# Kernel optimization log

Measured on AMD Instinct MI355X. Metric: run time of the kernel, lower is better.

Reference implementation:

```python
import jax, jax.numpy as jnp
import numpy as np

B, S, D, H = 2, 2048, 1024, 16
DK = D // H
SOFTCAP = 30.0


def setup_inputs() -> dict:
    key = jax.random.key(0)
    ks = jax.random.split(key, 6)
    inp = jax.random.normal(ks[0], (B, S, D), dtype=jnp.float32)
    count_bias = jax.random.normal(ks[1], (B, 1, S, S), dtype=jnp.float32) * 0.1
    # causal boolean mask: True = allowed
    causal = jnp.tril(jnp.ones((S, S), dtype=bool))
    attn_mask = jnp.broadcast_to(causal[None, None, :, :], (B, 1, S, S))
    scale = 0.02
    Wq = jax.random.normal(ks[2], (D, D), dtype=jnp.float32) * scale
    Wk = jax.random.normal(ks[3], (D, D), dtype=jnp.float32) * scale
    Wv = jax.random.normal(ks[4], (D, D), dtype=jnp.float32) * scale
    Wo = jax.random.normal(ks[5], (D, D), dtype=jnp.float32) * scale
    return {"inp": inp, "count_bias": count_bias, "attn_mask": attn_mask,
            "Wq": Wq, "Wk": Wk, "Wv": Wv, "Wo": Wo}


def reference(inp, count_bias, attn_mask, Wq, Wk, Wv, Wo):
    b = inp.shape[0]
    # nn.Linear: y = x @ W.T ; reshape to (B, H, S, DK)
    def proj(x, W):
        return jnp.einsum('bsd,ed->bse', x, W).reshape(b, -1, H, DK).transpose(0, 2, 1, 3)
    q = proj(inp, Wq)
    k = proj(inp, Wk)
    v = proj(inp, Wv)
    scale = 1.0 / np.sqrt(DK).astype(np.float32)
    scores = jnp.einsum('bhqd,bhkd->bhqk', q, k) * scale  # (B,H,S,S)
    scores = scores + count_bias  # broadcast over heads
    scores = jnp.tanh(scores / SOFTCAP) * SOFTCAP  # softcap > 0
    scores = jnp.where(attn_mask, scores, -jnp.inf)
    weights = jax.nn.softmax(scores, axis=-1)
    o = jnp.einsum('bhqk,bhkd->bhqd', weights, v)
    o = o.transpose(0, 2, 1, 3).reshape(b, -1, D)
    out = jnp.einsum('bsd,ed->bse', o, Wo)
    return out
```

## Files before the change

### kernel.cpp

```cpp
#include <hip/hip_runtime.h>
#include <hip/hip_bf16.h>

#define GK 1024

typedef __attribute__((ext_vector_type(8))) short bf16x8;
typedef __attribute__((ext_vector_type(4))) float f32x4;
typedef __attribute__((ext_vector_type(16))) float f32x16;
typedef __attribute__((ext_vector_type(4))) unsigned short ushort4v;

__device__ __forceinline__ f32x4 mfma16(bf16x8 a, bf16x8 b, f32x4 c) {
  return __builtin_amdgcn_mfma_f32_16x16x32_bf16(a, b, c, 0, 0, 0);
}
__device__ __forceinline__ f32x16 mfma32(bf16x8 a, bf16x8 b, f32x16 c) {
  return __builtin_amdgcn_mfma_f32_32x32x16_bf16(a, b, c, 0, 0, 0);
}

__device__ __forceinline__ unsigned short f2b(float f) {
  union { float f; unsigned int u; } x; x.f = f;
  return (unsigned short)((x.u + 0x7fffu + ((x.u >> 16) & 1u)) >> 16);
}

__device__ __forceinline__ unsigned int pk2(float lo, float hi) {
  float2 f; f.x = lo; f.y = hi;
  __hip_bfloat162 t = __float22bfloat162_rn(f);
  union { __hip_bfloat162 b; unsigned int u; } c; c.b = t;
  return c.u;
}

__device__ __forceinline__ float fexp2(float x) {
#if __has_builtin(__builtin_amdgcn_exp2f)
  return __builtin_amdgcn_exp2f(x);
#else
  return exp2f(x);
#endif
}
__device__ __forceinline__ float frcp(float x) {
#if __has_builtin(__builtin_amdgcn_rcpf)
  return __builtin_amdgcn_rcpf(x);
#else
  return 1.0f / x;
#endif
}

__device__ __forceinline__ void gl_lds16(const void* g, void* l) {
  __builtin_amdgcn_global_load_lds(
      (const __attribute__((address_space(1))) unsigned int*)g,
      (__attribute__((address_space(3))) unsigned int*)l, 16, 0, 0);
}

__global__ __launch_bounds__(256) void convert_kernel(
    const float* __restrict__ inp,
    const float* __restrict__ wq, const float* __restrict__ wk,
    const float* __restrict__ wv, const float* __restrict__ wo,
    unsigned short* __restrict__ Xb, unsigned short* __restrict__ Wcat)
{
  const size_t XN = (size_t)4194304;
  size_t i = ((size_t)blockIdx.x * 256 + threadIdx.x) * 4;
  const float* src; unsigned short* dst; size_t off;
  if (i < XN) {
    src = inp; dst = Xb; off = i;
  } else {
    size_t j = i - XN;
    int w = (int)(j >> 20);
    off = j & 1048575u;
    src = (w == 0) ? wq : (w == 1) ? wk : (w == 2) ? wv : wo;
    dst = Wcat + ((size_t)w << 20);
  }
  f32x4 v = *(const f32x4*)(src + off);
  ushort4v o;
#pragma unroll
  for (int t = 0; t < 4; ++t) o[t] = f2b(v[t]);
  *(ushort4v*)(dst + off) = o;
}

__device__ __forceinline__ void gemm_mainloop(
    const unsigned short* __restrict__ A, const unsigned short* __restrict__ Wt,
    int m0, int n0, int tid, unsigned short* As, unsigned short* Bs,
    f32x4 (&acc)[4][4])
{
  const int lane = tid & 63;
  const int wave = tid >> 6;
  const int wr = wave >> 1, wc = wave & 1;
  const int lq = lane & 15, g = lane >> 4;

  const int r_in = lane >> 2;
  const int c8 = (lane & 3) * 8;

  const unsigned short* Ap0 = A + (size_t)(m0 + wave * 32 + r_in) * GK + c8;
  const unsigned short* Ap1 = Ap0 + (size_t)16 * GK;
  const unsigned short* Wp0 = Wt + (size_t)(n0 + wave * 32 + r_in) * GK + c8;
  const unsigned short* Wp1 = Wp0 + (size_t)16 * GK;
  unsigned short* As0 = As + wave * 1024;
  unsigned short* Bs0 = Bs + wave * 1024;

  for (int kt = 0; kt < GK / 32; ++kt) {
    const int k0 = kt * 32;
    __syncthreads();
    gl_lds16(Ap0 + k0, As0);
    gl_lds16(Ap1 + k0, As0 + 512);
    gl_lds16(Wp0 + k0, Bs0);
    gl_lds16(Wp1 + k0, Bs0 + 512);
    __syncthreads();
    bf16x8 af[4], bfr[4];
#pragma unroll
    for (int i = 0; i < 4; ++i)
      af[i] = *(const bf16x8*)(As + (wr * 64 + i * 16 + lq) * 32 + g * 8);
#pragma unroll
    for (int j = 0; j < 4; ++j)
      bfr[j] = *(const bf16x8*)(Bs + (wc * 64 + j * 16 + lq) * 32 + g * 8);
#pragma unroll
    for (int i = 0; i < 4; ++i)
#pragma unroll
      for (int j = 0; j < 4; ++j)
        acc[i][j] = mfma16(af[i], bfr[j], acc[i][j]);
  }
}

__global__ __launch_bounds__(256) void gemm_qkv(
    const unsigned short* __restrict__ X, const unsigned short* __restrict__ Wcat,
    unsigned short* __restrict__ Qb, unsigned short* __restrict__ Kb,
    unsigned short* __restrict__ Vt)
{
  __shared__ unsigned short As[4096];
  __shared__ unsigned short Bs[4096];
  f32x4 acc[4][4];
#pragma unroll
  for (int i = 0; i < 4; ++i)
#pragma unroll
    for (int j = 0; j < 4; ++j) acc[i][j] = (f32x4){0.f, 0.f, 0.f, 0.f};

  const int z = blockIdx.z;
  const int m0 = blockIdx.x * 128, n0 = blockIdx.y * 128;
  gemm_mainloop(X, Wcat + ((size_t)z << 20), m0, n0, (int)threadIdx.x, As, Bs, acc);

  const int lane = threadIdx.x & 63;
  const int wave = threadIdx.x >> 6;
  const int wr = wave >> 1, wc = wave & 1, lq = lane & 15, g = lane >> 4;

  if (z < 2) {
    unsigned short* C = z ? Kb : Qb;
#pragma unroll
    for (int i = 0; i < 4; ++i)
#pragma unroll
      for (int j = 0; j < 4; ++j) {
        int col = n0 + wc * 64 + j * 16 + lq;
#pragma unroll
        for (int r = 0; r < 4; ++r) {
          int row = m0 + wr * 64 + i * 16 + g * 4 + r;
          C[(size_t)row * 1024 + col] = f2b(acc[i][j][r]);
        }
      }
  } else {
#pragma unroll
    for (int i = 0; i < 4; ++i)
#pragma unroll
      for (int j = 0; j < 4; ++j) {
        int col = n0 + wc * 64 + j * 16 + lq;
        int row0 = m0 + wr * 64 + i * 16 + g * 4;
        int b = row0 >> 11;
        int s = row0 & 2047;
        ushort4v pv;
#pragma unroll
        for (int r = 0; r < 4; ++r) pv[r] = f2b(acc[i][j][r]);
        *(ushort4v*)(Vt + (size_t)(b * 1024 + col) * 2048 + s) = pv;
      }
  }
}

__global__ __launch_bounds__(256) void gemm_out(
    const unsigned short* __restrict__ Ob, const unsigned short* __restrict__ Wo,
    float* __restrict__ out)
{
  __shared__ unsigned short As[4096];
  __shared__ unsigned short Bs[4096];
  f32x4 acc[4][4];
#pragma unroll
  for (int i = 0; i < 4; ++i)
#pragma unroll
    for (int j = 0; j < 4; ++j) acc[i][j] = (f32x4){0.f, 0.f, 0.f, 0.f};

  const int m0 = blockIdx.x * 128, n0 = blockIdx.y * 128;
  gemm_mainloop(Ob, Wo, m0, n0, (int)threadIdx.x, As, Bs, acc);

  const int lane = threadIdx.x & 63;
  const int wave = threadIdx.x >> 6;
  const int wr = wave >> 1, wc = wave & 1, lq = lane & 15, g = lane >> 4;
#pragma unroll
  for (int i = 0; i < 4; ++i)
#pragma unroll
    for (int j = 0; j < 4; ++j) {
      int col = n0 + wc * 64 + j * 16 + lq;
#pragma unroll
      for (int r = 0; r < 4; ++r) {
        int row = m0 + wr * 64 + i * 16 + g * 4 + r;
        out[(size_t)row * 1024 + col] = acc[i][j][r];
      }
    }
}

__device__ __forceinline__ void attn_chain(
    const bf16x8 (&qf)[4], const f32x4 (&bvs)[4],
    bf16x8 kf0, bf16x8 kf1, bf16x8 kf2, bf16x8 kf3,
    bf16x8 va00, bf16x8 va01, bf16x8 va10, bf16x8 va11,
    bool msk, int ql, int hi,
    f32x16& o0, f32x16& o1, float& pls)
{
  const float INV30 = 0.033333333333f;
  const float C3 = -0.333333333f, C5 = 0.133333333f;
  const float C1 = 43.28085122666891f;

  f32x16 st = {0.f,0.f,0.f,0.f,0.f,0.f,0.f,0.f,0.f,0.f,0.f,0.f,0.f,0.f,0.f,0.f};
  st = mfma32(kf0, qf[0], st);
  st = mfma32(kf1, qf[1], st);
  st = mfma32(kf2, qf[2], st);
  st = mfma32(kf3, qf[3], st);

  float p[16];
#pragma unroll
  for (int reg = 0; reg < 16; ++reg) {
    float v = fmaf(st[reg], 0.125f, bvs[reg >> 2][reg & 3]);
    float y = v * INV30;
    float y2 = y * y;
    float t = y * fmaf(y2, fmaf(y2, C5, C3), 1.0f);
    p[reg] = fexp2(fmaf(t, C1, -C1));
  }
  if (msk) {
#pragma unroll
    for (int reg = 0; reg < 16; ++reg) {
      int krow = (reg & 3) + 8 * (reg >> 2) + 4 * hi;
      p[reg] = (krow <= ql) ? p[reg] : 0.f;
    }
  }
  float a0 = (p[0] + p[1]) + (p[2] + p[3]);
  float a1 = (p[4] + p[5]) + (p[6] + p[7]);
  float a2 = (p[8] + p[9]) + (p[10] + p[11]);
  float a3 = (p[12] + p[13]) + (p[14] + p[15]);
  pls += (a0 + a1) + (a2 + a3);

  unsigned int wv[8];
#pragma unroll
  for (int j = 0; j < 8; ++j) wv[j] = pk2(p[2 * j], p[2 * j + 1]);
  unsigned int x0 = hi ? wv[0] : wv[2], x1 = hi ? wv[1] : wv[3];
  x0 = __shfl_xor(x0, 32); x1 = __shfl_xor(x1, 32);
  unsigned int y0 = hi ? wv[4] : wv[6], y1 = hi ? wv[5] : wv[7];
  y0 = __shfl_xor(y0, 32); y1 = __shfl_xor(y1, 32);
  union { unsigned int u[4]; bf16x8 v; } B0, B1;
  B0.u[0] = hi ? x0 : wv[0]; B0.u[1] = hi ? x1 : wv[1];
  B0.u[2] = hi ? wv[2] : x0; B0.u[3] = hi ? wv[3] : x1;
  B1.u[0] = hi ? y0 : wv[4]; B1.u[1] = hi ? y1 : wv[5];
  B1.u[2] = hi ? wv[6] : y0; B1.u[3] = hi ? wv[7] : y1;

  o0 = mfma32(va00, B0.v, o0);
  o0 = mfma32(va01, B1.v, o0);
  o1 = mfma32(va10, B0.v, o1);
  o1 = mfma32(va11, B1.v, o1);
}

__global__ __launch_bounds__(256, 2) void attn_fwd(
    const unsigned short* __restrict__ Qb, const unsigned short* __restrict__ Kb,
    const unsigned short* __restrict__ Vt, const float* __restrict__ bias,
    unsigned short* __restrict__ Ob)
{
  __shared__ __attribute__((aligned(16))) unsigned char lds[65536];

  const int tid = (int)threadIdx.x;
  const int lane = tid & 63;
  const int w = tid >> 6;
  const int bid = (int)blockIdx.x;
  const int bh = (bid & 7) * 4 + ((bid >> 3) & 3);
  const int qp = bid >> 5;
  const int b = bh >> 4, h = bh & 15;
  const int tA = qp, tB = 63 - qp;
  const int q0A = tA * 32, q0B = tB * 32;
  const int ql = lane & 31;
  const int hi = lane >> 5;

  const unsigned short* QpA = Qb + (size_t)(b * 2048 + q0A + ql) * 1024 + h * 64 + 8 * hi;
  const unsigned short* QpB = Qb + (size_t)(b * 2048 + q0B + ql) * 1024 + h * 64 + 8 * hi;
  bf16x8 qfA[4], qfB[4];
#pragma unroll
  for (int c = 0; c < 4; ++c) {
    qfA[c] = *(const bf16x8*)(QpA + 16 * c);
    qfB[c] = *(const bf16x8*)(QpB + 16 * c);
  }

  const unsigned short* KsrcL = Kb + (size_t)(b * 2048 + (lane >> 3)) * 1024
                                + h * 64 + (((lane & 7) ^ ((lane >> 3) & 7)) << 3);
  const unsigned short* VsrcL = Vt + (size_t)(bh * 64 + (lane >> 2)) * 2048
                                + (((lane & 3) ^ ((lane >> 2) & 3)) << 3);
  unsigned char* const KdstW = lds + w * 16384;

  const float* BpA = bias + (size_t)b * 4194304 + (size_t)(q0A + ql) * 2048 + 4 * hi;
  const float* BpB = bias + (size_t)b * 4194304 + (size_t)(q0B + ql) * 2048 + 4 * hi;

  float plsA = 0.f, plsB = 0.f;
  f32x16 oA0 = {0.f,0.f,0.f,0.f,0.f,0.f,0.f,0.f,0.f,0.f,0.f,0.f,0.f,0.f,0.f,0.f};
  f32x16 oA1 = oA0, oB0 = oA0, oB1 = oA0;

  auto stageKV = [&](int kt, int db) {
    unsigned char* Kd = KdstW + db * 8192;
    unsigned char* Vd = Kd + 4096;
#pragma unroll
    for (int j = 0; j < 4; ++j)
      gl_lds16(KsrcL + (size_t)kt * 32768 + j * 8192, Kd + j * 1024);
#pragma unroll
    for (int j = 0; j < 4; ++j)
      gl_lds16(VsrcL + (size_t)j * 32768 + kt * 32, Vd + j * 1024);
  };

  stageKV(w, 0);
  int db = 0;
  for (int kt = w; kt <= tB; kt += 4) {
    const bool doA = (kt <= tA);
    f32x4 bvsB[4], bvsA[4];
#pragma unroll
    for (int j = 0; j < 4; ++j) bvsB[j] = *(const f32x4*)(BpB + kt * 32 + 8 * j);
    if (doA) {
#pragma unroll
      for (int j = 0; j < 4; ++j) bvsA[j] = *(const f32x4*)(BpA + kt * 32 + 8 * j);
    }
    __builtin_amdgcn_sched_barrier(0);
    const bool hasNext = (kt + 4 <= tB);
    if (hasNext) {
      stageKV(kt + 4, db ^ 1);
      asm volatile("s_waitcnt vmcnt(8)" ::: "memory");
    } else {
      asm volatile("s_waitcnt vmcnt(0)" ::: "memory");
    }
    __builtin_amdgcn_sched_barrier(0);

    const unsigned char* Ksh = KdstW + db * 8192;
    const unsigned char* Vsh = Ksh + 4096;
    bf16x8 kf[4];
#pragma unroll
    for (int c = 0; c < 4; ++c)
      kf[c] = *(const bf16x8*)(Ksh + ql * 128 + (((hi + 2 * c) ^ (ql & 7)) << 4));
    const int vb = ((ql >> 4) << 10) + ((ql & 15) << 6);
    bf16x8 va00 = *(const bf16x8*)(Vsh + vb + (((hi) ^ (ql & 3)) << 4));
    bf16x8 va01 = *(const bf16x8*)(Vsh + vb + (((hi + 2) ^ (ql & 3)) << 4));
    bf16x8 va10 = *(const bf16x8*)(Vsh + 2048 + vb + (((hi) ^ (ql & 3)) << 4));
    bf16x8 va11 = *(const bf16x8*)(Vsh + 2048 + vb + (((hi + 2) ^ (ql & 3)) << 4));

    attn_chain(qfB, bvsB, kf[0], kf[1], kf[2], kf[3], va00, va01, va10, va11,
               kt == tB, ql, hi, oB0, oB1, plsB);
    if (doA) {
      attn_chain(qfA, bvsA, kf[0], kf[1], kf[2], kf[3], va00, va01, va10, va11,
                 kt == tA, ql, hi, oA0, oA1, plsA);
    }
    db ^= 1;
  }

  __syncthreads();
  float* ldsF = (float*)lds;
  float* lsumbuf = ldsF + 8448;
  float* rowinv = ldsF + 8960;
  lsumbuf[(w * 2 + hi) * 32 + ql] = plsA;
  lsumbuf[256 + (w * 2 + hi) * 32 + ql] = plsB;
  if (w >= 2) {
    float* OA = ldsF + (w - 2) * 2112;
    float* OB = ldsF + (2 + (w - 2)) * 2112;
#pragma unroll
    for (int reg = 0; reg < 16; ++reg) {
      int d0 = (reg & 3) + 8 * (reg >> 2) + 4 * hi;
      OA[d0 * 33 + ql] = oA0[reg];
      OA[(d0 + 32) * 33 + ql] = oA1[reg];
      OB[d0 * 33 + ql] = oB0[reg];
      OB[(d0 + 32) * 33 + ql] = oB1[reg];
    }
  }
  __syncthreads();
  if (w < 2) {
    float* OA = ldsF + w * 2112;
    float* OB = ldsF + (2 + w) * 2112;
#pragma unroll
    for (int reg = 0; reg < 16; ++reg) {
      int d0 = (reg & 3) + 8 * (reg >> 2) + 4 * hi;
      OA[d0 * 33 + ql] += oA0[reg];
      OA[(d0 + 32) * 33 + ql] += oA1[reg];
      OB[d0 * 33 + ql] += oB0[reg];
      OB[(d0 + 32) * 33 + ql] += oB1[reg];
    }
  }
  __syncthreads();
  if (tid < 64) {
    int t = tid >> 5, q = tid & 31;
    float s = 0.f;
#pragma unroll
    for (int j = 0; j < 8; ++j) s += lsumbuf[t * 256 + j * 32 + q];
    rowinv[t * 32 + q] = frcp(s);
  }
  __syncthreads();
#pragma unroll
  for (int it = 0; it < 16; ++it) {
    int i = it * 256 + tid;
    int t = i >> 11;
    int rem = i & 2047;
    int q = rem >> 6, d = rem & 63;
    float val = (ldsF[t * 4224 + d * 33 + q] + ldsF[t * 4224 + 2112 + d * 33 + q])
                * rowinv[t * 32 + q];
    int row = b * 2048 + (t ? q0B : q0A) + q;
    Ob[(size_t)row * 1024 + h * 64 + d] = f2b(val);
  }
}

extern "C" void kernel_launch(void* const* d_in, const int* in_sizes, int n_in,
                              void* d_out, int out_size, void* d_ws, size_t ws_size,
                              hipStream_t stream) {
  (void)in_sizes; (void)n_in; (void)out_size; (void)ws_size;
  const float* inp  = (const float*)d_in[0];
  const float* bias = (const float*)d_in[1];
  const float* wq = (const float*)d_in[3];
  const float* wk = (const float*)d_in[4];
  const float* wv = (const float*)d_in[5];
  const float* wo = (const float*)d_in[6];
  float* out = (float*)d_out;

  unsigned short* Xb   = (unsigned short*)d_ws;
  unsigned short* Wcat = Xb + 4194304;
  unsigned short* Qb   = Wcat + 4194304;
  unsigned short* Kb   = Qb + 4194304;
  unsigned short* Vt   = Kb + 4194304;
  unsigned short* Ob   = Vt + 4194304;

  convert_kernel<<<8192, 256, 0, stream>>>(inp, wq, wk, wv, wo, Xb, Wcat);
  gemm_qkv<<<dim3(32, 8, 3), dim3(256), 0, stream>>>(Xb, Wcat, Qb, Kb, Vt);
  attn_fwd<<<1024, 256, 0, stream>>>(Qb, Kb, Vt, bias, Ob);
  gemm_out<<<dim3(32, 8, 1), dim3(256), 0, stream>>>(Ob, Wcat + 3 * 1048576, out);
}
```

Before: 146.4 us.

## Process two KV tiles per warp iteration instead of double-buffered prefetch

Replaces the software-pipelined loop with a different schedule. Before, each warp prefetched the next K/V tile into a second LDS buffer while it computed on the current one. Now each warp stages two consecutive K/V tiles and their bias values at once, waits for all loads, then runs the attention chain on both tiles in turn. This puts more memory requests in flight per wait and cuts loop overhead, but it gives up the overlap between loading and compute. It may also stage a tile one past the causal limit without using it, a read that can go out of bounds.

```diff
diff --git a/kernel.cpp b/kernel.cpp
--- a/kernel.cpp
+++ b/kernel.cpp
@@ -288,7 +288,7 @@
                                 + h * 64 + (((lane & 7) ^ ((lane >> 3) & 7)) << 3);
   const unsigned short* VsrcL = Vt + (size_t)(bh * 64 + (lane >> 2)) * 2048
                                 + (((lane & 3) ^ ((lane >> 2) & 3)) << 3);
-  unsigned char* const KdstW = lds + w * 16384;
+  unsigned char* const Kdst = lds + w * 16384;
 
   const float* BpA = bias + (size_t)b * 4194304 + (size_t)(q0A + ql) * 2048 + 4 * hi;
   const float* BpB = bias + (size_t)b * 4194304 + (size_t)(q0B + ql) * 2048 + 4 * hi;
@@ -297,8 +297,8 @@
   f32x16 oA0 = {0.f,0.f,0.f,0.f,0.f,0.f,0.f,0.f,0.f,0.f,0.f,0.f,0.f,0.f,0.f,0.f};
   f32x16 oA1 = oA0, oB0 = oA0, oB1 = oA0;
 
-  auto stageKV = [&](int kt, int db) {
-    unsigned char* Kd = KdstW + db * 8192;
+  auto stageKV = [&](int kt, int off) {
+    unsigned char* Kd = Kdst + off;
     unsigned char* Vd = Kd + 4096;
 #pragma unroll
     for (int j = 0; j < 4; ++j)
@@ -307,47 +307,65 @@
     for (int j = 0; j < 4; ++j)
       gl_lds16(VsrcL + (size_t)j * 32768 + kt * 32, Vd + j * 1024);
   };
-
-  stageKV(w, 0);
-  int db = 0;
-  for (int kt = w; kt <= tB; kt += 4) {
-    const bool doA = (kt <= tA);
-    f32x4 bvsB[4], bvsA[4];
-#pragma unroll
-    for (int j = 0; j < 4; ++j) bvsB[j] = *(const f32x4*)(BpB + kt * 32 + 8 * j);
-    if (doA) {
-#pragma unroll
-      for (int j = 0; j < 4; ++j) bvsA[j] = *(const f32x4*)(BpA + kt * 32 + 8 * j);
-    }
-    __builtin_amdgcn_sched_barrier(0);
-    const bool hasNext = (kt + 4 <= tB);
-    if (hasNext) {
-      stageKV(kt + 4, db ^ 1);
-      asm volatile("s_waitcnt vmcnt(8)" ::: "memory");
-    } else {
-      asm volatile("s_waitcnt vmcnt(0)" ::: "memory");
-    }
-    __builtin_amdgcn_sched_barrier(0);
-
-    const unsigned char* Ksh = KdstW + db * 8192;
+  auto ldfrags = [&](int off, bf16x8 (&kf)[4], bf16x8& va00, bf16x8& va01,
+                     bf16x8& va10, bf16x8& va11) {
+    const unsigned char* Ksh = Kdst + off;
     const unsigned char* Vsh = Ksh + 4096;
-    bf16x8 kf[4];
 #pragma unroll
     for (int c = 0; c < 4; ++c)
       kf[c] = *(const bf16x8*)(Ksh + ql * 128 + (((hi + 2 * c) ^ (ql & 7)) << 4));
     const int vb = ((ql >> 4) << 10) + ((ql & 15) << 6);
-    bf16x8 va00 = *(const bf16x8*)(Vsh + vb + (((hi) ^ (ql & 3)) << 4));
-    bf16x8 va01 = *(const bf16x8*)(Vsh + vb + (((hi + 2) ^ (ql & 3)) << 4));
-    bf16x8 va10 = *(const bf16x8*)(Vsh + 2048 + vb + (((hi) ^ (ql & 3)) << 4));
-    bf16x8 va11 = *(const bf16x8*)(Vsh + 2048 + vb + (((hi + 2) ^ (ql & 3)) << 4));
-
-    attn_chain(qfB, bvsB, kf[0], kf[1], kf[2], kf[3], va00, va01, va10, va11,
-               kt == tB, ql, hi, oB0, oB1, plsB);
-    if (doA) {
-      attn_chain(qfA, bvsA, kf[0], kf[1], kf[2], kf[3], va00, va01, va10, va11,
-                 kt == tA, ql, hi, oA0, oA1, plsA);
-    }
-    db ^= 1;
+    va00 = *(const bf16x8*)(Vsh + vb + (((hi) ^ (ql & 3)) << 4));
+    va01 = *(const bf16x8*)(Vsh + vb + (((hi + 2) ^ (ql & 3)) << 4));
+    va10 = *(const bf16x8*)(Vsh + 2048 + vb + (((hi) ^ (ql & 3)) << 4));
+    va11 = *(const bf16x8*)(Vsh + 2048 + vb + (((hi + 2) ^ (ql & 3)) << 4));
+  };
+
+  for (int kt0 = 2 * w; kt0 <= tB; kt0 += 8) {
+    const int kt1 = kt0 + 1;
+    const bool doB1 = (kt1 <= tB);
+    const bool doA0 = (kt0 <= tA);
+    const bool doA1 = (kt1 <= tA);
+
+    __builtin_amdgcn_sched_barrier(0);
+    stageKV(kt0, 0);
+    stageKV(kt1, 8192);
+    f32x4 bB0[4], bB1[4], bA0[4], bA1[4];
+#pragma unroll
+    for (int j = 0; j < 4; ++j) bB0[j] = *(const f32x4*)(BpB + kt0 * 32 + 8 * j);
+    if (doB1) {
+#pragma unroll
+      for (int j = 0; j < 4; ++j) bB1[j] = *(const f32x4*)(BpB + kt1 * 32 + 8 * j);
+    }
+    if (doA0) {
+#pragma unroll
+      for (int j = 0; j < 4; ++j) bA0[j] = *(const f32x4*)(BpA + kt0 * 32 + 8 * j);
+    }
+    if (doA1) {
+#pragma unroll
+      for (int j = 0; j < 4; ++j) bA1[j] = *(const f32x4*)(BpA + kt1 * 32 + 8 * j);
+    }
+    asm volatile("s_waitcnt vmcnt(0)" ::: "memory");
+    __builtin_amdgcn_sched_barrier(0);
+
+    {
+      bf16x8 kf[4], va00, va01, va10, va11;
+      ldfrags(0, kf, va00, va01, va10, va11);
+      attn_chain(qfB, bB0, kf[0], kf[1], kf[2], kf[3], va00, va01, va10, va11,
+                 kt0 == tB, ql, hi, oB0, oB1, plsB);
+      if (doA0)
+        attn_chain(qfA, bA0, kf[0], kf[1], kf[2], kf[3], va00, va01, va10, va11,
+                   kt0 == tA, ql, hi, oA0, oA1, plsA);
+    }
+    if (doB1) {
+      bf16x8 kf[4], va00, va01, va10, va11;
+      ldfrags(8192, kf, va00, va01, va10, va11);
+      attn_chain(qfB, bB1, kf[0], kf[1], kf[2], kf[3], va00, va01, va10, va11,
+                 kt1 == tB, ql, hi, oB0, oB1, plsB);
+      if (doA1)
+        attn_chain(qfA, bA1, kf[0], kf[1], kf[2], kf[3], va00, va01, va10, va11,
+                   kt1 == tA, ql, hi, oA0, oA1, plsA);
+    }
   }
 
   __syncthreads();
```

New measurement: 142.4 us. -2.7%, faster.
